# Performance work log

Measured on AMD Instinct MI355X. Metric: run time of the kernel, lower is better.

Reference implementation:

```python
import jax, jax.numpy as jnp
import numpy as np

N = 100_000   # nodes
E = 1_600_000 # edges (avg degree 16)
D = 128       # in_dim
H = 128       # hidden_dim


def _glorot(key, shape):
    s = 1.0 / np.sqrt(shape[0])
    return jax.random.uniform(key, shape, jnp.float32, -s, s)


def setup_inputs() -> dict:
    key = jax.random.key(0)
    ks = jax.random.split(key, 8)
    x = jax.random.normal(ks[0], (N, D), jnp.float32)
    edge_index = jax.random.randint(ks[1], (2, E), 0, N)
    return {
        "x": x,
        "edge_index": edge_index,
        "Wn0": _glorot(ks[2], (D, H)),
        "Wr0": _glorot(ks[3], (D, H)),
        "b0": jnp.zeros((H,), jnp.float32),
        "Wn1": _glorot(ks[4], (H, H)),
        "Wr1": _glorot(ks[5], (H, H)),
        "b1": jnp.zeros((H,), jnp.float32),
        "Wh": _glorot(ks[6], (H, 1)),
        "bh": jnp.zeros((1,), jnp.float32),
    }


def _mean_agg(h, src, dst, n):
    # mean of source-node features scattered onto destination nodes
    summed = jax.ops.segment_sum(h[src], dst, num_segments=n)  # [N, F]
    cnt = jax.ops.segment_sum(jnp.ones((src.shape[0],), h.dtype), dst,
                              num_segments=n)
    return summed / jnp.maximum(cnt, 1.0)[:, None]


def _sage_layer(h, src, dst, Wn, Wr, b):
    # PyG SAGEConv (mean aggr): lin_l(mean_neighbors) + lin_r(root) + bias
    agg = _mean_agg(h, src, dst, h.shape[0])
    return agg @ Wn + h @ Wr + b


def reference(x, edge_index, Wn0, Wr0, b0, Wn1, Wr1, b1, Wh, bh):
    src, dst = edge_index[0], edge_index[1]
    h = jax.nn.relu(_sage_layer(x, src, dst, Wn0, Wr0, b0))  # dropout = identity (eval)
    h = jax.nn.relu(_sage_layer(h, src, dst, Wn1, Wr1, b1))
    logits = (h @ Wh + bh)[:, 0]  # squeeze(-1) -> [N]
    return logits
```

## Files before the change

kernel.cpp:

```cpp
#include <hip/hip_runtime.h>

#define THREADS 256
#define SCAN_ITEMS 8
#define NSB 128
#define BKT_MAX 3200
#define CHUNK 1024

typedef float f32x4 __attribute__((ext_vector_type(4)));
typedef float floatx2 __attribute__((ext_vector_type(2)));
typedef __bf16 bf16x8 __attribute__((ext_vector_type(8)));
typedef int intx4 __attribute__((ext_vector_type(4)));

__device__ inline unsigned short f32_to_bf16_rne(float f) {
    unsigned int u = __float_as_uint(f);
    unsigned int r = u + 0x7fffu + ((u >> 16) & 1u);
    return (unsigned short)(r >> 16);
}
__device__ inline float bf16_bits_to_f32(unsigned short h) {
    return __uint_as_float(((unsigned int)h) << 16);
}
__device__ inline uint4 pack8(const unsigned short* s) {
    uint4 u;
    u.x = (unsigned int)s[0] | ((unsigned int)s[1] << 16);
    u.y = (unsigned int)s[2] | ((unsigned int)s[3] << 16);
    u.z = (unsigned int)s[4] | ((unsigned int)s[5] << 16);
    u.w = (unsigned int)s[6] | ((unsigned int)s[7] << 16);
    return u;
}
__device__ inline unsigned int pk_fp8(float a, float b) {
    return (unsigned int)__builtin_amdgcn_cvt_pk_fp8_f32(a, b, 0, false);
}
__device__ inline floatx2 unpk_fp8(unsigned int u) {
    return __builtin_amdgcn_cvt_pk_f32_fp8(u, false);
}

__global__ __launch_bounds__(256) void prep(
    const int* __restrict__ dst, int* __restrict__ hist, int E, int nbkt, int chunk,
    const float4* __restrict__ x4, unsigned int* __restrict__ xq4, int n4,
    const float* __restrict__ Wn0, const float* __restrict__ Wr0, uint4* __restrict__ Wsw0,
    const float* __restrict__ Wn1, const float* __restrict__ Wr1, uint4* __restrict__ Wsw1) {
    __shared__ int lh[BKT_MAX];
    const int tid = threadIdx.x, blk = blockIdx.x;
    if (blk < NSB) {
        for (int i = tid; i < nbkt; i += 256) lh[i] = 0;
        __syncthreads();
        int s = blk * chunk, e = s + chunk; if (e > E) e = E;
        int n4e = (e > s) ? ((e - s) >> 2) : 0;
        const intx4* d4p = (const intx4*)(dst + s);
        for (int i = tid; i < n4e; i += 256) {
            intx4 d4 = d4p[i];
#pragma unroll
            for (int k = 0; k < 4; k++) atomicAdd(&lh[d4[k] >> 5], 1);
        }
        for (int j = s + (n4e << 2) + tid; j < e; j += 256) atomicAdd(&lh[dst[j] >> 5], 1);
        __syncthreads();
        for (int i = tid; i < nbkt; i += 256) hist[i * NSB + blk] = lh[i];
    } else if (blk < NSB + 32) {
        int b2 = blk - NSB;
        const float* Wn = (b2 < 16) ? Wn0 : Wn1;
        const float* Wr = (b2 < 16) ? Wr0 : Wr1;
        uint4* out = (b2 < 16) ? Wsw0 : Wsw1;
        int id = (b2 & 15) * 256 + tid;
        int lane = id & 63;
        int nt = (id >> 6) & 7;
        int t = id >> 9;
        int kbase = t * 32 + (lane >> 4) * 8;
        int col = nt * 16 + (lane & 15);
        unsigned short hi[8], lo[8];
#pragma unroll
        for (int j = 0; j < 8; j++) {
            int k = kbase + j;
            const float* W = (k < 128) ? (Wn + (size_t)k * 128) : (Wr + (size_t)(k - 128) * 128);
            float v = W[col];
            unsigned short h = f32_to_bf16_rne(v);
            hi[j] = h;
            lo[j] = f32_to_bf16_rne(v - bf16_bits_to_f32(h));
        }
        out[(size_t)((t * 8 + nt) * 2 + 0) * 64 + lane] = pack8(hi);
        out[(size_t)((t * 8 + nt) * 2 + 1) * 64 + lane] = pack8(lo);
    } else {
        int i = (blk - NSB - 32) * 256 + tid;
        if (i < n4) {
            float4 v = x4[i];
            unsigned int u = pk_fp8(v.x, v.y);
            u |= (unsigned int)__builtin_amdgcn_cvt_pk_fp8_f32(v.z, v.w, 0, false) << 16;
            xq4[i] = u;
        }
    }
}

__global__ void scan1_kernel(const int* __restrict__ cnt, int* __restrict__ off,
                             int* __restrict__ bsums, int n) {
    __shared__ int sdata[THREADS];
    int base = blockIdx.x * (THREADS * SCAN_ITEMS) + threadIdx.x * SCAN_ITEMS;
    int vals[SCAN_ITEMS];
    int tsum = 0;
#pragma unroll
    for (int k = 0; k < SCAN_ITEMS; k++) {
        int idx = base + k;
        int v = (idx < n) ? cnt[idx] : 0;
        vals[k] = tsum;
        tsum += v;
    }
    sdata[threadIdx.x] = tsum;
    __syncthreads();
    for (int s = 1; s < THREADS; s <<= 1) {
        int y = (threadIdx.x >= (unsigned)s) ? sdata[threadIdx.x - s] : 0;
        __syncthreads();
        sdata[threadIdx.x] += y;
        __syncthreads();
    }
    int texcl = sdata[threadIdx.x] - tsum;
#pragma unroll
    for (int k = 0; k < SCAN_ITEMS; k++) {
        int idx = base + k;
        if (idx < n) off[idx] = texcl + vals[k];
    }
    if (threadIdx.x == THREADS - 1) bsums[blockIdx.x] = sdata[THREADS - 1];
}

__global__ void scan2_wave(const int* __restrict__ bsums, int* __restrict__ bbase,
                           int nb, int* __restrict__ offN) {
    const int lane = threadIdx.x;
    int carry = 0;
    for (int base = 0; base < nb; base += 64) {
        int i = base + lane;
        int v = (i < nb) ? bsums[i] : 0;
        int x = v;
#pragma unroll
        for (int s = 1; s < 64; s <<= 1) {
            int y = __shfl_up(x, s);
            if (lane >= s) x += y;
        }
        if (i < nb) bbase[i] = carry + x - v;
        carry += __shfl(x, 63);
    }
    if (lane == 0) *offN = carry;
}

__global__ __launch_bounds__(256) void scatter32(const int* __restrict__ src,
                                                 const int* __restrict__ dst,
                                                 const int* __restrict__ hstS,
                                                 const int* __restrict__ bbase,
                                                 int* __restrict__ esrt,
                                                 int E, int nbkt, int chunk) {
    __shared__ int cur[BKT_MAX];
    const int tid = threadIdx.x, blk = blockIdx.x;
    for (int i = tid; i < nbkt; i += 256) {
        int j = i * NSB + blk;
        cur[i] = hstS[j] + bbase[j >> 11];
    }
    __syncthreads();
    int s = blk * chunk, e = s + chunk; if (e > E) e = E;
    if ((((size_t)dst | (size_t)src) & 15) == 0) {
        int n4 = (e > s) ? ((e - s) >> 2) : 0;
        const intx4* d4p = (const intx4*)(dst + s);
        const intx4* s4p = (const intx4*)(src + s);
        for (int i = tid; i < n4; i += 256) {
            intx4 d4 = d4p[i];
            intx4 s4 = s4p[i];
#pragma unroll
            for (int k = 0; k < 4; k++) {
                int d = d4[k];
                int p = atomicAdd(&cur[d >> 5], 1);
                esrt[p] = (s4[k] << 7) | ((d & 31) << 25);
            }
        }
        for (int j = s + (n4 << 2) + tid; j < e; j += 256) {
            int d = dst[j];
            int p = atomicAdd(&cur[d >> 5], 1);
            esrt[p] = (src[j] << 7) | ((d & 31) << 25);
        }
    } else {
        for (int j = s + tid; j < e; j += 256) {
            int d = dst[j];
            int p = atomicAdd(&cur[d >> 5], 1);
            esrt[p] = (src[j] << 7) | ((d & 31) << 25);
        }
    }
}

__global__ __launch_bounds__(256) void agg_bucket(const unsigned char* __restrict__ hb,
                                                  const int* __restrict__ hstS,
                                                  const int* __restrict__ bbase,
                                                  const int* __restrict__ esrt,
                                                  unsigned short* __restrict__ aggb,
                                                  int E, int nbkt, int n) {
    __shared__ int stage[CHUNK];
    __shared__ int sorted[CHUNK];
    __shared__ int cnt[32];
    __shared__ int coff[33];
    const int tid = threadIdx.x, lane = tid & 63, w = tid >> 6;
    const int b = blockIdx.x;

    int j0 = b * NSB;
    const int p0 = hstS[j0] + bbase[j0 >> 11];
    int p1 = E;
    if (b + 1 < nbkt) {
        int j1 = (b + 1) * NSB;
        p1 = hstS[j1] + bbase[j1 >> 11];
    }
    const char* hbB = (const char*)hb;

    if (p1 - p0 <= CHUNK) {
        int m = p1 - p0;
        for (int i = tid; i < m; i += 256) stage[i] = esrt[p0 + i];
        if (tid < 32) cnt[tid] = 0;
        __syncthreads();
        for (int i = tid; i < m; i += 256) atomicAdd(&cnt[stage[i] >> 25], 1);
        __syncthreads();
        if (tid < 32) {
            int v = cnt[tid];
            int x = v;
#pragma unroll
            for (int s = 1; s < 32; s <<= 1) {
                int y = __shfl_up(x, s);
                if (lane >= s) x += y;
            }
            coff[tid + 1] = x;
            if (tid == 0) coff[0] = 0;
            cnt[tid] = x - v;
        }
        __syncthreads();
        for (int i = tid; i < m; i += 256) {
            int pk = stage[i];
            int p = atomicAdd(&cnt[pk >> 25], 1);
            sorted[p] = pk;
        }
        __syncthreads();

        int no[9];
#pragma unroll
        for (int i = 0; i <= 8; i++) no[i] = coff[w * 8 + i];
        const int s = no[0], e2 = no[8];
        const int w8 = w * 8;
        int curL = 0;
        float ax = 0.f, ay = 0.f;

        auto flushTo = [&](int tgt) {
            while (curL < tgt) {
                int node = b * 32 + w8 + curL;
                int d = no[curL + 1] - no[curL];
                float inv = 1.0f / (float)(d > 1 ? d : 1);
                unsigned int o = (unsigned int)f32_to_bf16_rne(ax * inv)
                               | ((unsigned int)f32_to_bf16_rne(ay * inv) << 16);
                if (node < n)
                    *(unsigned int*)((char*)aggb + (size_t)node * 256 + lane * 4) = o;
                ax = 0.f; ay = 0.f; ++curL;
            }
        };
        auto issue = [&](unsigned int* v, int* nd, int base) {
#pragma unroll
            for (int j = 0; j < 8; j++) {
                int pk = sorted[base + j];
                nd[j] = (pk >> 25) - w8;
                v[j] = *(const unsigned short*)(hbB + (unsigned)(pk & 0x00FFFF80) + lane * 2);
            }
        };
        auto consume = [&](const unsigned int* v, const int* nd) {
#pragma unroll
            for (int j = 0; j < 8; j++) {
                flushTo(nd[j]);
                floatx2 f = unpk_fp8(v[j]);
                ax += f.x;
                ay += f.y;
            }
        };

        const int nb8 = (e2 - s) >> 3;
        unsigned int vA[8], vB[8];
        int ndA[8], ndB[8];
        if (nb8 > 0) {
            issue(vA, ndA, s);
            int k = 1;
            for (; k + 1 < nb8; k += 2) {
                issue(vB, ndB, s + k * 8);
                consume(vA, ndA);
                issue(vA, ndA, s + k * 8 + 8);
                consume(vB, ndB);
            }
            if (k < nb8) {
                issue(vB, ndB, s + k * 8);
                consume(vA, ndA);
                consume(vB, ndB);
            } else {
                consume(vA, ndA);
            }
        }
        for (int i = s + (nb8 << 3); i < e2; i++) {
            int pk = sorted[i];
            flushTo((pk >> 25) - w8);
            unsigned int vv = *(const unsigned short*)(hbB + (unsigned)(pk & 0x00FFFF80) + lane * 2);
            floatx2 f = unpk_fp8(vv);
            ax += f.x;
            ay += f.y;
        }
        flushTo(8);
        return;
    }

    float accx[8], accy[8];
    int dcnt[8];
#pragma unroll
    for (int nl = 0; nl < 8; nl++) { accx[nl] = 0.f; accy[nl] = 0.f; dcnt[nl] = 0; }
    for (int base = p0; base < p1; base += CHUNK) {
        int m = p1 - base; if (m > CHUNK) m = CHUNK;
        for (int i = tid; i < m; i += 256) stage[i] = esrt[base + i];
        if (tid < 32) cnt[tid] = 0;
        __syncthreads();
        for (int i = tid; i < m; i += 256) atomicAdd(&cnt[stage[i] >> 25], 1);
        __syncthreads();
        if (tid < 32) {
            int v = cnt[tid];
            int x = v;
#pragma unroll
            for (int s = 1; s < 32; s <<= 1) {
                int y = __shfl_up(x, s);
                if (lane >= s) x += y;
            }
            coff[tid + 1] = x;
            if (tid == 0) coff[0] = 0;
            cnt[tid] = x - v;
        }
        __syncthreads();
        for (int i = tid; i < m; i += 256) {
            int pk = stage[i];
            int p = atomicAdd(&cnt[pk >> 25], 1);
            sorted[p] = pk;
        }
        __syncthreads();
#pragma unroll
        for (int nl = 0; nl < 8; nl++) {
            int node_l = w * 8 + nl;
            int s = coff[node_l], e2 = coff[node_l + 1];
            dcnt[nl] += e2 - s;
            float ax = accx[nl], ay = accy[nl];
            int i = s;
            for (; i + 8 <= e2; i += 8) {
                unsigned int v[8];
#pragma unroll
                for (int j = 0; j < 8; j++) {
                    unsigned off = (unsigned)(sorted[i + j] & 0x00FFFF80);
                    v[j] = *(const unsigned short*)(hbB + off + lane * 2);
                }
#pragma unroll
                for (int j = 0; j < 8; j++) {
                    floatx2 f = unpk_fp8(v[j]);
                    ax += f.x;
                    ay += f.y;
                }
            }
            for (; i < e2; i++) {
                unsigned off = (unsigned)(sorted[i] & 0x00FFFF80);
                unsigned int vv = *(const unsigned short*)(hbB + off + lane * 2);
                floatx2 f = unpk_fp8(vv);
                ax += f.x;
                ay += f.y;
            }
            accx[nl] = ax; accy[nl] = ay;
        }
        __syncthreads();
    }
#pragma unroll
    for (int nl = 0; nl < 8; nl++) {
        int node = b * 32 + w * 8 + nl;
        if (node < n) {
            int d = dcnt[nl];
            float inv = 1.0f / (float)(d > 1 ? d : 1);
            unsigned int o = (unsigned int)f32_to_bf16_rne(accx[nl] * inv)
                           | ((unsigned int)f32_to_bf16_rne(accy[nl] * inv) << 16);
            *(unsigned int*)(aggb + (size_t)node * 128 + lane * 2) = o;
        }
    }
}

template <int LAYER, bool FINAL>
__global__ __launch_bounds__(256, 2) void update_mfma(
    const unsigned short* __restrict__ aggb, const void* __restrict__ hsrc,
    const uint4* __restrict__ Wsw, const float* __restrict__ bias,
    unsigned short* __restrict__ hout, unsigned char* __restrict__ houtq,
    const float* __restrict__ Wh, const float* __restrict__ bh,
    float* __restrict__ logits, int n) {
    __shared__ uint4 Alds[2048];
    __shared__ uint4 Wlds[2048];
    const int tid = threadIdx.x;
    const int lane = tid & 63;
    const int w = tid >> 6;
    const int i0 = blockIdx.x * 128;

    f32x4 acc[2][8];
#pragma unroll
    for (int mt = 0; mt < 2; mt++)
#pragma unroll
        for (int nt = 0; nt < 8; nt++) acc[mt][nt] = (f32x4)0.f;

    const int r = tid >> 1;
    const int half = tid & 1;
    const int rg = i0 + r;
    const bool inb = rg < n;
    const int mt_s = r >> 4;
    const int lidx = r & 15;

    for (int c = 0; c < 4; c++) {
        const bool haslo = (LAYER == 0 && c >= 2);
        {
            const uint4* srcW = Wsw + (size_t)c * 2048;
#pragma unroll
            for (int g = 0; g < 8; g++) Wlds[g * 256 + tid] = srcW[g * 256 + tid];
        }
        {
            unsigned short hiA[32], loA[32];
            if (LAYER == 0 && c >= 2) {
                const float4* s4 = (const float4*)((const float*)hsrc + (size_t)rg * 128 +
                                                   (c - 2) * 64 + half * 32);
#pragma unroll
                for (int q = 0; q < 8; q++) {
                    float4 f = inb ? s4[q] : make_float4(0.f, 0.f, 0.f, 0.f);
                    float vv[4] = {f.x, f.y, f.z, f.w};
#pragma unroll
                    for (int e = 0; e < 4; e++) {
                        unsigned short h = f32_to_bf16_rne(vv[e]);
                        hiA[q * 4 + e] = h;
                        loA[q * 4 + e] = f32_to_bf16_rne(vv[e] - bf16_bits_to_f32(h));
                    }
                }
            } else {
                const unsigned short* bsrc = (c < 2) ? aggb : (const unsigned short*)hsrc;
                int cc = (c < 2) ? c : c - 2;
                const uint4* s4 = (const uint4*)(bsrc + (size_t)rg * 128 + cc * 64 + half * 32);
#pragma unroll
                for (int q = 0; q < 4; q++) {
                    uint4 u = inb ? s4[q] : make_uint4(0, 0, 0, 0);
                    unsigned int uu[4] = {u.x, u.y, u.z, u.w};
#pragma unroll
                    for (int e = 0; e < 4; e++) {
                        hiA[q * 8 + e * 2 + 0] = (unsigned short)(uu[e] & 0xffffu);
                        hiA[q * 8 + e * 2 + 1] = (unsigned short)(uu[e] >> 16);
                    }
                }
            }
            unsigned int baseHi = ((mt_s * 2 + half) * 2 + 0) * 64;
#pragma unroll
            for (int g2 = 0; g2 < 4; g2++)
                Alds[baseHi + lidx + 16 * g2] = pack8(&hiA[g2 * 8]);
            if (haslo) {
#pragma unroll
                for (int g2 = 0; g2 < 4; g2++)
                    Alds[baseHi + 64 + lidx + 16 * g2] = pack8(&loA[g2 * 8]);
            }
        }
        __syncthreads();
#pragma unroll
        for (int kt = 0; kt < 2; kt++) {
            bf16x8 a0h = *(const bf16x8*)&Alds[(((w * 2 + 0) * 2 + kt) * 2 + 0) * 64 + lane];
            bf16x8 a1h = *(const bf16x8*)&Alds[(((w * 2 + 1) * 2 + kt) * 2 + 0) * 64 + lane];
            bf16x8 a0l, a1l;
            if (haslo) {
                a0l = *(const bf16x8*)&Alds[(((w * 2 + 0) * 2 + kt) * 2 + 1) * 64 + lane];
                a1l = *(const bf16x8*)&Alds[(((w * 2 + 1) * 2 + kt) * 2 + 1) * 64 + lane];
            }
#pragma unroll
            for (int nt = 0; nt < 8; nt++) {
                bf16x8 bhv = *(const bf16x8*)&Wlds[((kt * 8 + nt) * 2 + 0) * 64 + lane];
                bf16x8 blv = *(const bf16x8*)&Wlds[((kt * 8 + nt) * 2 + 1) * 64 + lane];
                acc[0][nt] = __builtin_amdgcn_mfma_f32_16x16x32_bf16(a0h, bhv, acc[0][nt], 0, 0, 0);
                acc[0][nt] = __builtin_amdgcn_mfma_f32_16x16x32_bf16(a0h, blv, acc[0][nt], 0, 0, 0);
                acc[1][nt] = __builtin_amdgcn_mfma_f32_16x16x32_bf16(a1h, bhv, acc[1][nt], 0, 0, 0);
                acc[1][nt] = __builtin_amdgcn_mfma_f32_16x16x32_bf16(a1h, blv, acc[1][nt], 0, 0, 0);
                if (haslo) {
                    acc[0][nt] = __builtin_amdgcn_mfma_f32_16x16x32_bf16(a0l, bhv, acc[0][nt], 0, 0, 0);
                    acc[1][nt] = __builtin_amdgcn_mfma_f32_16x16x32_bf16(a1l, bhv, acc[1][nt], 0, 0, 0);
                }
            }
        }
        __syncthreads();
    }

    const int col = lane & 15;
    const int g4 = lane >> 4;
    float bcol[8];
#pragma unroll
    for (int nt = 0; nt < 8; nt++) bcol[nt] = bias[nt * 16 + col];
    if (!FINAL) {
#pragma unroll
        for (int mt = 0; mt < 2; mt++) {
            int nodeBase = i0 + (w * 2 + mt) * 16 + g4 * 4;
#pragma unroll
            for (int reg = 0; reg < 4; reg++) {
                int node = nodeBase + reg;
                if (node < n) {
#pragma unroll
                    for (int nt = 0; nt < 8; nt++) {
                        float v = acc[mt][nt][reg] + bcol[nt];
                        v = v > 0.f ? v : 0.f;
                        hout[(size_t)node * 128 + nt * 16 + col] = f32_to_bf16_rne(v);
                        houtq[(size_t)node * 128 + nt * 16 + col] =
                            (unsigned char)(pk_fp8(v, v) & 0xffu);
                    }
                }
            }
        }
    } else {
        float whc[8];
#pragma unroll
        for (int nt = 0; nt < 8; nt++) whc[nt] = Wh[nt * 16 + col];
        float bhv = bh[0];
#pragma unroll
        for (int mt = 0; mt < 2; mt++) {
            int nodeBase = i0 + (w * 2 + mt) * 16 + g4 * 4;
#pragma unroll
            for (int reg = 0; reg < 4; reg++) {
                float s = 0.f;
#pragma unroll
                for (int nt = 0; nt < 8; nt++) {
                    float v = acc[mt][nt][reg] + bcol[nt];
                    v = v > 0.f ? v : 0.f;
                    s += v * whc[nt];
                }
                s += __shfl_xor(s, 1);
                s += __shfl_xor(s, 2);
                s += __shfl_xor(s, 4);
                s += __shfl_xor(s, 8);
                int node = nodeBase + reg;
                if (col == 0 && node < n) logits[node] = s + bhv;
            }
        }
    }
}

extern "C" void kernel_launch(void* const* d_in, const int* in_sizes, int n_in,
                              void* d_out, int out_size, void* d_ws, size_t ws_size,
                              hipStream_t stream) {
    const float* x   = (const float*)d_in[0];
    const int*   ei  = (const int*)d_in[1];
    const float* Wn0 = (const float*)d_in[2];
    const float* Wr0 = (const float*)d_in[3];
    const float* b0  = (const float*)d_in[4];
    const float* Wn1 = (const float*)d_in[5];
    const float* Wr1 = (const float*)d_in[6];
    const float* b1  = (const float*)d_in[7];
    const float* Wh  = (const float*)d_in[8];
    const float* bh  = (const float*)d_in[9];
    float* logits = (float*)d_out;

    int N = in_sizes[0] / 128;
    int E = in_sizes[1] / 2;
    const int* src = ei;
    const int* dst = ei + E;

    int nbkt = (N + 31) >> 5;
    int HS = nbkt * NSB;
    int NB = (HS + 2047) / 2048;
    int chunk = (((E + NSB - 1) / NSB) + 3) & ~3;

    char* ws = (char*)d_ws;
    size_t cur = 0;
    auto alloc = [&](size_t bytes) -> void* {
        void* p = ws + cur;
        cur += (bytes + 255) & ~(size_t)255;
        return p;
    };
    int* hist  = (int*)alloc((size_t)HS * 4);
    int* bsums = (int*)alloc((size_t)NB * 4);
    int* bbase = (int*)alloc((size_t)NB * 4);
    int* scrat = (int*)alloc(256);
    int* esrt  = (int*)alloc((size_t)E * 4);
    unsigned char* xq  = (unsigned char*)alloc((size_t)N * 128);
    unsigned char* h0q = (unsigned char*)alloc((size_t)N * 128);
    unsigned short* h0b = (unsigned short*)alloc((size_t)N * 128 * 2);
    unsigned short* agb = (unsigned short*)alloc((size_t)N * 128 * 2);
    uint4* Wsw0 = (uint4*)alloc(131072);
    uint4* Wsw1 = (uint4*)alloc(131072);
    (void)ws_size; (void)n_in; (void)out_size;

    int n4 = N * 32;
    int gPrep = NSB + 32 + (n4 + 255) / 256;
    hipLaunchKernelGGL(prep, dim3(gPrep), dim3(256), 0, stream,
                       dst, hist, E, nbkt, chunk,
                       (const float4*)x, (unsigned int*)xq, n4,
                       Wn0, Wr0, Wsw0, Wn1, Wr1, Wsw1);

    hipLaunchKernelGGL(scan1_kernel,  dim3(NB),  dim3(256), 0, stream, hist, hist, bsums, HS);
    hipLaunchKernelGGL(scan2_wave,    dim3(1),   dim3(64),  0, stream, bsums, bbase, NB, scrat);
    hipLaunchKernelGGL(scatter32,     dim3(NSB), dim3(256), 0, stream, src, dst, hist, bbase, esrt, E, nbkt, chunk);

    int gUpd = (N + 127) / 128;

    hipLaunchKernelGGL(agg_bucket, dim3(nbkt), dim3(256), 0, stream, xq, hist, bbase, esrt, agb, E, nbkt, N);
    hipLaunchKernelGGL((update_mfma<0, false>), dim3(gUpd), dim3(256), 0, stream,
                       agb, (const void*)x, Wsw0, b0, h0b, h0q, nullptr, nullptr, nullptr, N);
    hipLaunchKernelGGL(agg_bucket, dim3(nbkt), dim3(256), 0, stream, h0q, hist, bbase, esrt, agb, E, nbkt, N);
    hipLaunchKernelGGL((update_mfma<1, true>), dim3(gUpd), dim3(256), 0, stream,
                       agb, (const void*)h0b, Wsw1, b1, nullptr, nullptr, Wh, bh, logits, N);
}
```

Before: 298.3 us.

## Split wavefront into half-waves gathering two edges per load in fast aggregation path

In the main aggregation path each wavefront now processes two edges per load. The low 32 lanes read the even edge's row and the high 32 lanes the odd edge's row, each lane loading 4 fp8 bytes instead of 2. Partial sums are combined across the halves with a shuffle at flush time, and node ids are made wave-uniform with readfirstlane. The aim is to halve the number of gather instructions and use wider loads, at the cost of extra shuffles and divergent branching when the two edges of a pair belong to different nodes. The fallback path's unrolled 8-way gather loop is replaced by a simple scalar loop that now reads through hb rather than hbB.

```diff
diff --git a/kernel.cpp b/kernel.cpp
--- a/kernel.cpp
+++ b/kernel.cpp
@@ -30,8 +30,11 @@
 __device__ inline unsigned int pk_fp8(float a, float b) {
     return (unsigned int)__builtin_amdgcn_cvt_pk_fp8_f32(a, b, 0, false);
 }
-__device__ inline floatx2 unpk_fp8(unsigned int u) {
+__device__ inline floatx2 unpk_fp8_lo(unsigned int u) {
     return __builtin_amdgcn_cvt_pk_f32_fp8(u, false);
+}
+__device__ inline floatx2 unpk_fp8_hi(unsigned int u) {
+    return __builtin_amdgcn_cvt_pk_f32_fp8(u, true);
 }
 
 __global__ __launch_bounds__(256) void prep(
@@ -234,66 +237,87 @@
         for (int i = 0; i <= 8; i++) no[i] = coff[w * 8 + i];
         const int s = no[0], e2 = no[8];
         const int w8 = w * 8;
+        const int l32 = lane & 31;
+        const bool hiH = lane >= 32;
         int curL = 0;
-        float ax = 0.f, ay = 0.f;
+        floatx2 a01 = (floatx2)0.f, a23 = (floatx2)0.f;
 
         auto flushTo = [&](int tgt) {
             while (curL < tgt) {
+                float t0 = a01.x + __shfl_xor(a01.x, 32);
+                float t1 = a01.y + __shfl_xor(a01.y, 32);
+                float t2 = a23.x + __shfl_xor(a23.x, 32);
+                float t3 = a23.y + __shfl_xor(a23.y, 32);
                 int node = b * 32 + w8 + curL;
                 int d = no[curL + 1] - no[curL];
                 float inv = 1.0f / (float)(d > 1 ? d : 1);
-                unsigned int o = (unsigned int)f32_to_bf16_rne(ax * inv)
-                               | ((unsigned int)f32_to_bf16_rne(ay * inv) << 16);
-                if (node < n)
-                    *(unsigned int*)((char*)aggb + (size_t)node * 256 + lane * 4) = o;
-                ax = 0.f; ay = 0.f; ++curL;
+                if (!hiH && node < n) {
+                    uint2 o;
+                    o.x = (unsigned int)f32_to_bf16_rne(t0 * inv)
+                        | ((unsigned int)f32_to_bf16_rne(t1 * inv) << 16);
+                    o.y = (unsigned int)f32_to_bf16_rne(t2 * inv)
+                        | ((unsigned int)f32_to_bf16_rne(t3 * inv) << 16);
+                    *(uint2*)((char*)aggb + (size_t)node * 256 + l32 * 8) = o;
+                }
+                a01 = (floatx2)0.f; a23 = (floatx2)0.f;
+                ++curL;
             }
         };
-        auto issue = [&](unsigned int* v, int* nd, int base) {
-#pragma unroll
-            for (int j = 0; j < 8; j++) {
-                int pk = sorted[base + j];
-                nd[j] = (pk >> 25) - w8;
-                v[j] = *(const unsigned short*)(hbB + (unsigned)(pk & 0x00FFFF80) + lane * 2);
-            }
+        auto accum = [&](unsigned int v) {
+            a01 += unpk_fp8_lo(v);
+            a23 += unpk_fp8_hi(v);
         };
-        auto consume = [&](const unsigned int* v, const int* nd) {
-#pragma unroll
-            for (int j = 0; j < 8; j++) {
-                flushTo(nd[j]);
-                floatx2 f = unpk_fp8(v[j]);
-                ax += f.x;
-                ay += f.y;
+        auto issueP = [&](unsigned int* v, int* ndE, int* ndO, int base) {
+#pragma unroll
+            for (int j = 0; j < 4; j++) {
+                int kEv = sorted[base + 2 * j];
+                int kOv = sorted[base + 2 * j + 1];
+                ndE[j] = (__builtin_amdgcn_readfirstlane(kEv) >> 25) - w8;
+                ndO[j] = (__builtin_amdgcn_readfirstlane(kOv) >> 25) - w8;
+                int kSel = hiH ? kOv : kEv;
+                v[j] = *(const unsigned int*)(hbB + (unsigned)(kSel & 0x00FFFF80) + l32 * 4);
             }
         };
+        auto consumeP = [&](const unsigned int* v, const int* ndE, const int* ndO) {
+#pragma unroll
+            for (int j = 0; j < 4; j++) {
+                if (ndE[j] == ndO[j]) {
+                    flushTo(ndE[j]);
+                    accum(v[j]);
+                } else {
+                    flushTo(ndE[j]);
+                    if (!hiH) accum(v[j]);
+                    flushTo(ndO[j]);
+                    if (hiH) accum(v[j]);
+                }
+            }
+        };
 
         const int nb8 = (e2 - s) >> 3;
-        unsigned int vA[8], vB[8];
-        int ndA[8], ndB[8];
+        unsigned int vA[4], vB[4];
+        int neA[4], noA[4], neB[4], noB[4];
         if (nb8 > 0) {
-            issue(vA, ndA, s);
+            issueP(vA, neA, noA, s);
             int k = 1;
             for (; k + 1 < nb8; k += 2) {
-                issue(vB, ndB, s + k * 8);
-                consume(vA, ndA);
-                issue(vA, ndA, s + k * 8 + 8);
-                consume(vB, ndB);
+                issueP(vB, neB, noB, s + k * 8);
+                consumeP(vA, neA, noA);
+                issueP(vA, neA, noA, s + k * 8 + 8);
+                consumeP(vB, neB, noB);
             }
             if (k < nb8) {
-                issue(vB, ndB, s + k * 8);
-                consume(vA, ndA);
-                consume(vB, ndB);
+                issueP(vB, neB, noB, s + k * 8);
+                consumeP(vA, neA, noA);
+                consumeP(vB, neB, noB);
             } else {
-                consume(vA, ndA);
+                consumeP(vA, neA, noA);
             }
         }
         for (int i = s + (nb8 << 3); i < e2; i++) {
-            int pk = sorted[i];
-            flushTo((pk >> 25) - w8);
-            unsigned int vv = *(const unsigned short*)(hbB + (unsigned)(pk & 0x00FFFF80) + lane * 2);
-            floatx2 f = unpk_fp8(vv);
-            ax += f.x;
-            ay += f.y;
+            int k = __builtin_amdgcn_readfirstlane(sorted[i]);
+            flushTo((k >> 25) - w8);
+            unsigned int vv = *(const unsigned int*)(hbB + (unsigned)(k & 0x00FFFF80) + l32 * 4);
+            if (!hiH) accum(vv);
         }
         flushTo(8);
         return;
@@ -335,25 +359,10 @@
             int s = coff[node_l], e2 = coff[node_l + 1];
             dcnt[nl] += e2 - s;
             float ax = accx[nl], ay = accy[nl];
-            int i = s;
-            for (; i + 8 <= e2; i += 8) {
-                unsigned int v[8];
-#pragma unroll
-                for (int j = 0; j < 8; j++) {
-                    unsigned off = (unsigned)(sorted[i + j] & 0x00FFFF80);
-                    v[j] = *(const unsigned short*)(hbB + off + lane * 2);
-                }
-#pragma unroll
-                for (int j = 0; j < 8; j++) {
-                    floatx2 f = unpk_fp8(v[j]);
-                    ax += f.x;
-                    ay += f.y;
-                }
-            }
-            for (; i < e2; i++) {
+            for (int i = s; i < e2; i++) {
                 unsigned off = (unsigned)(sorted[i] & 0x00FFFF80);
-                unsigned int vv = *(const unsigned short*)(hbB + off + lane * 2);
-                floatx2 f = unpk_fp8(vv);
+                unsigned int vv = *(const unsigned short*)((const char*)hb + off + lane * 2);
+                floatx2 f = unpk_fp8_lo(vv);
                 ax += f.x;
                 ay += f.y;
             }
```

New measurement: 326.2 us. +9.3%, slower.
